# Kernel tuning notes

Measured on AMD Instinct MI355X. Metric: run time of the kernel, lower is better.

Reference implementation:

```python
import jax, jax.numpy as jnp
import numpy as np
import math

L, H, P = 16384, 128, 256


def setup_inputs() -> dict:
    key = jax.random.key(0)
    k = jax.random.split(key, 6)
    return {
        "input_sequence": jax.random.normal(k[0], (L, H), dtype=jnp.float32),
        "A_diag": jax.random.uniform(k[1], (P,), dtype=jnp.float32),
        "B": (jax.random.uniform(k[2], (P, H, 2), dtype=jnp.float32) * 2.0 - 1.0) / math.sqrt(H),
        "C": (jax.random.uniform(k[3], (H, P, 2), dtype=jnp.float32) * 2.0 - 1.0) / math.sqrt(P),
        "D": jax.random.normal(k[4], (H,), dtype=jnp.float32),
        "steps": jax.random.uniform(k[5], (P,), dtype=jnp.float32),
    }


def _binop(qi, qj):
    # 2x2 block-diagonal matrix product + affine state propagation, per channel.
    iA, iB, iC, iD, ib1, ib2 = qi
    jA, jB, jC, jD, jb1, jb2 = qj
    return (
        jA * iA + jB * iC,
        jA * iB + jB * iD,
        jC * iA + jD * iC,
        jC * iB + jD * iD,
        jA * ib1 + jB * ib2 + jb1,
        jC * ib1 + jD * ib2 + jb2,
    )


def reference(input_sequence, A_diag, B, C, D, steps):
    # LinOSS-IM discretization (implicit)
    A = jax.nn.relu(A_diag)                      # (P,)
    dt = jax.nn.sigmoid(steps)                   # (P,)
    Bc = B[..., 0] + 1j * B[..., 1]              # (P,H) complex64
    Cc = C[..., 0] + 1j * C[..., 1]              # (H,P) complex64

    Bu = input_sequence @ Bc.T                   # (L,P) complex64

    schur = 1.0 / (1.0 + dt ** 2 * A)
    M11 = 1.0 - dt ** 2 * A * schur
    M12 = -dt * A * schur
    M21 = dt * schur
    M22 = schur

    ones = jnp.ones((input_sequence.shape[0], A.shape[0]), dtype=input_sequence.dtype)
    F1 = M11 * Bu * dt                           # (L,P) complex
    F2 = M21 * Bu * dt

    elems = (M11 * ones, M12 * ones, M21 * ones, M22 * ones, F1, F2)
    _, _, _, _, _, x2 = jax.lax.associative_scan(_binop, elems)  # scan over L

    ys = jnp.real(x2 @ Cc.T)                     # (L,H)
    return ys + input_sequence * D
```

## Files before the change

### kernel.cpp

```cpp
#include <hip/hip_runtime.h>
#include <math.h>

#define L 16384
#define H 128
#define P 256
#define CL 32
#define NCH (L/CL)
#define GS 16
#define NG (NCH/GS)
#define KDIM 512
#define NBU 512

#define SENT 0xFFC0DEADFFC0DEADULL
#define SENT_WORDS (2*NCH*P + 2*NG*P)

typedef __attribute__((ext_vector_type(8))) short short8;
typedef __attribute__((ext_vector_type(4))) float f32x4;

__device__ inline unsigned short f2bf(float f){
  union { float f; unsigned u; } v; v.f = f;
  unsigned u = v.u;
  u += 0x7fffu + ((u >> 16) & 1u);
  return (unsigned short)(u >> 16);
}
__device__ inline float bf2f(unsigned short s){
  union { unsigned u; float f; } v; v.u = ((unsigned)s) << 16;
  return v.f;
}

struct Params { float M11,M12,M21,M22,s1,s2; };

__device__ inline Params get_params(const float* A_diag, const float* steps, int p){
  float A = A_diag[p]; A = A > 0.f ? A : 0.f;
  float dt = 1.f/(1.f + expf(-steps[p]));
  float schur = 1.f/(1.f + dt*dt*A);
  Params q;
  q.M11 = 1.f - dt*dt*A*schur;
  q.M12 = -dt*A*schur;
  q.M21 = dt*schur;
  q.M22 = schur;
  q.s1 = q.M11*dt;
  q.s2 = q.M21*dt;
  return q;
}

__device__ inline unsigned long long aload(const unsigned long long* p){
  return __hip_atomic_load((unsigned long long*)p, __ATOMIC_RELAXED,
                           __HIP_MEMORY_SCOPE_AGENT);
}
__device__ inline void apub(unsigned long long* p, unsigned long long v){
  (void)__hip_atomic_exchange(p, v, __ATOMIC_RELAXED, __HIP_MEMORY_SCOPE_AGENT);
}

__global__ __launch_bounds__(512) void prep_w(const float* __restrict__ B,
                                              const float* __restrict__ Cw,
                                              unsigned short* __restrict__ BWswz,
                                              unsigned short* __restrict__ Bswz,
                                              unsigned long long* __restrict__ sent){
  int gidx = blockIdx.x*512 + threadIdx.x;
  sent[gidx] = SENT;
  if (gidx < H*NBU){
    int k = gidx >> 9, n = gidx & 511;
    int p = n & 255, c2 = n >> 8;
    float v = B[((size_t)p*H + k)*2 + c2];
    BWswz[((size_t)(k>>3)*NBU + n)*8 + (k&7)] = f2bf(v);
  } else if (gidx < 2*H*NBU){
    int g2 = gidx - H*NBU;
    int k = g2 >> 7, n = g2 & 127;
    float v = (k < P) ? Cw[((size_t)n*P + k)*2]
                      : -Cw[((size_t)n*P + (k-P))*2 + 1];
    Bswz[((size_t)(k>>3)*H + n)*8 + (k&7)] = f2bf(v);
  }
}

__global__ __launch_bounds__(512, 4) void linoss_fused(
    const float* __restrict__ in,
    const float* __restrict__ A_diag,
    const float* __restrict__ steps,
    const float* __restrict__ Dv,
    const unsigned short* __restrict__ BWswz,
    const unsigned short* __restrict__ Bswz,
    unsigned long long* __restrict__ finals,
    unsigned long long* __restrict__ gfin,
    float* __restrict__ out)
{
  __shared__ unsigned short sX[CL][NBU+8];
  const int c   = blockIdx.x;
  const int tid = threadIdx.x;

  {
    int lane = tid & 63, w = tid >> 6;
    int ml = lane & 15, quad = lane >> 4;
    int mt = w & 1, ng = w >> 1;
    int lm0 = mt*16;
    const float* aptr = in + (size_t)(c*CL + lm0 + ml)*H + quad*8;
    short8 av[4];
    #pragma unroll
    for (int ks=0; ks<4; ks++){
      float4 f0 = *(const float4*)(aptr + ks*32);
      float4 f1 = *(const float4*)(aptr + ks*32 + 4);
      union { short8 s; unsigned short u[8]; } o;
      o.u[0]=f2bf(f0.x); o.u[1]=f2bf(f0.y); o.u[2]=f2bf(f0.z); o.u[3]=f2bf(f0.w);
      o.u[4]=f2bf(f1.x); o.u[5]=f2bf(f1.y); o.u[6]=f2bf(f1.z); o.u[7]=f2bf(f1.w);
      av[ks] = o.s;
    }
    f32x4 acc[8];
    #pragma unroll
    for (int t=0;t<8;t++) acc[t] = (f32x4){0.f,0.f,0.f,0.f};
    #pragma unroll
    for (int ks=0; ks<4; ks++){
      #pragma unroll
      for (int t=0;t<8;t++){
        int n0 = (ng*8 + t)*16;
        short8 bv = *(const short8*)(BWswz + ((size_t)(ks*4+quad)*NBU + n0 + ml)*8);
        acc[t] = __builtin_amdgcn_mfma_f32_16x16x32_bf16(av[ks], bv, acc[t], 0, 0, 0);
      }
    }
    #pragma unroll
    for (int t=0;t<8;t++){
      int n = (ng*8+t)*16 + ml;
      #pragma unroll
      for (int r=0;r<4;r++)
        sX[lm0 + quad*4 + r][n] = f2bf(acc[t][r]);
    }
  }
  __syncthreads();

  const int p = tid & 255, part = tid >> 8;
  Params q = get_params(A_diag, steps, p);
  float Ta=q.M11, Tb=q.M12, Tc=q.M21, Td=q.M22;
  #pragma unroll
  for (int s=0;s<5;s++){
    float na=Ta*Ta+Tb*Tc, nb=Ta*Tb+Tb*Td, nc=Tc*Ta+Td*Tc, nd=Tc*Tb+Td*Td;
    Ta=na;Tb=nb;Tc=nc;Td=nd;
  }
  float fx1=0.f, fx2=0.f;
  {
    #pragma unroll
    for (int i=0;i<CL;i++){
      float u = bf2f(sX[i][part*256 + p]);
      float n1 = q.M11*fx1 + q.M12*fx2 + q.s1*u;
      float n2 = q.M21*fx1 + q.M22*fx2 + q.s2*u;
      fx1 = n1; fx2 = n2;
    }
    union { unsigned long long u; float2 f; } w; w.f = make_float2(fx1,fx2);
    apub(&finals[(size_t)(part*NCH + c)*P + p], w.u);
  }

  const int g = c >> 4, iw = c & (GS-1);
  const unsigned long long* Fp = finals + (size_t)part*NCH*P + (size_t)g*GS*P + p;

  float z1=0.f, z2v=0.f;
  bool have_z = false;
  if (iw == GS-1){
    unsigned long long v[GS-1];
    #pragma unroll
    for (int j=0;j<GS-1;j++) v[j] = aload(Fp + (size_t)j*P);
    #pragma unroll
    for (int j=0;j<GS-1;j++){
      while (v[j]==SENT){ __builtin_amdgcn_s_sleep(2); v[j] = aload(Fp + (size_t)j*P); }
    }
    #pragma unroll
    for (int j=0;j<GS-1;j++){
      union { unsigned long long u; float2 f; } w; w.u = v[j];
      float n1 = Ta*z1 + Tb*z2v + w.f.x;
      float n2 = Tc*z1 + Td*z2v + w.f.y;
      z1=n1; z2v=n2;
    }
    have_z = true;
    float t1 = Ta*z1 + Tb*z2v + fx1;
    float t2 = Tc*z1 + Td*z2v + fx2;
    union { unsigned long long u; float2 f; } w; w.f = make_float2(t1,t2);
    apub(&gfin[(size_t)(part*NG + g)*P + p], w.u);
  }

  {
    float sa=1.f, sb=0.f, sc=0.f, sd=1.f;
    {
      float wa=Ta, wb=Tb, wc=Tc, wd=Td;
      #pragma unroll
      for (int bit=0; bit<4; bit++){
        if ((iw>>bit)&1){
          float na = wa*sa + wb*sc, nb = wa*sb + wb*sd;
          float nc = wc*sa + wd*sc, nd = wc*sb + wd*sd;
          sa=na; sb=nb; sc=nc; sd=nd;
        }
        float qa = wa*wa + wb*wc, qb = wa*wb + wb*wd;
        float qc = wc*wa + wd*wc, qd = wc*wb + wd*wd;
        wa=qa; wb=qb; wc=qc; wd=qd;
      }
    }
    float ga=Ta, gb=Tb, gc=Tc, gd=Td;
    #pragma unroll
    for (int s=0;s<4;s++){
      float na=ga*ga+gb*gc, nb=ga*gb+gb*gd, nc=gc*ga+gd*gc, nd=gc*gb+gd*gd;
      ga=na;gb=nb;gc=nc;gd=nd;
    }
    float y1=0.f, y2=0.f;
    {
      const unsigned long long* Gp = gfin + (size_t)part*NG*P + p;
      for (int t0=0; t0<NG-1 && t0<g; t0+=8){
        unsigned long long v[8];
        #pragma unroll
        for (int j=0;j<8;j++){
          int jj = t0+j;
          v[j] = (jj < g) ? aload(Gp + (size_t)jj*P) : 0ULL;
        }
        #pragma unroll
        for (int j=0;j<8;j++){
          int jj = t0+j;
          if (jj < g){
            while (v[j]==SENT){ __builtin_amdgcn_s_sleep(2); v[j] = aload(Gp + (size_t)jj*P); }
          }
        }
        #pragma unroll
        for (int j=0;j<8;j++){
          int jj = t0+j;
          if (jj < g){
            union { unsigned long long u; float2 f; } w; w.u = v[j];
            float n1 = ga*y1 + gb*y2 + w.f.x;
            float n2 = gc*y1 + gd*y2 + w.f.y;
            y1=n1; y2=n2;
          }
        }
      }
    }
    if (!have_z){
      for (int t0=0; t0<GS-1 && t0<iw; t0+=8){
        unsigned long long v[8];
        #pragma unroll
        for (int j=0;j<8;j++){
          int jj = t0+j;
          v[j] = (jj < iw) ? aload(Fp + (size_t)jj*P) : 0ULL;
        }
        #pragma unroll
        for (int j=0;j<8;j++){
          int jj = t0+j;
          if (jj < iw){
            while (v[j]==SENT){ __builtin_amdgcn_s_sleep(2); v[j] = aload(Fp + (size_t)jj*P); }
          }
        }
        #pragma unroll
        for (int j=0;j<8;j++){
          int jj = t0+j;
          if (jj < iw){
            union { unsigned long long u; float2 f; } w; w.u = v[j];
            float n1 = Ta*z1 + Tb*z2v + w.f.x;
            float n2 = Tc*z1 + Td*z2v + w.f.y;
            z1=n1; z2v=n2;
          }
        }
      }
    }
    float x1 = sa*y1 + sb*y2 + z1;
    float x2 = sc*y1 + sd*y2 + z2v;
    #pragma unroll
    for (int i=0;i<CL;i++){
      float u = bf2f(sX[i][part*256 + p]);
      float n1 = q.M11*x1 + q.M12*x2 + q.s1*u;
      float n2 = q.M21*x1 + q.M22*x2 + q.s2*u;
      x1 = n1; x2 = n2;
      sX[i][part*256 + p] = f2bf(x2);
    }
  }
  __syncthreads();

  {
    int lane = tid & 63, w = tid >> 6;
    int ml = lane & 15, quad = lane >> 4;
    int mt = w & 1;
    int ntb = (w >> 1) * 2;
    f32x4 acc[2];
    acc[0] = (f32x4){0.f,0.f,0.f,0.f};
    acc[1] = (f32x4){0.f,0.f,0.f,0.f};
    for (int ks=0; ks<KDIM/32; ks++){
      short8 av = *(const short8*)&sX[mt*16 + ml][ks*32 + quad*8];
      #pragma unroll
      for (int j=0;j<2;j++){
        short8 bv = *(const short8*)(Bswz + ((size_t)(ks*4+quad)*H + (ntb+j)*16 + ml)*8);
        acc[j] = __builtin_amdgcn_mfma_f32_16x16x32_bf16(av, bv, acc[j], 0, 0, 0);
      }
    }
    #pragma unroll
    for (int j=0;j<2;j++){
      int h = (ntb+j)*16 + ml;
      float dv = Dv[h];
      #pragma unroll
      for (int r=0;r<4;r++){
        int l = c*CL + mt*16 + quad*4 + r;
        out[(size_t)l*H + h] = acc[j][r] + in[(size_t)l*H + h]*dv;
      }
    }
  }
}

extern "C" void kernel_launch(void* const* d_in, const int* in_sizes, int n_in,
                              void* d_out, int out_size, void* d_ws, size_t ws_size,
                              hipStream_t stream) {
  const float* in     = (const float*)d_in[0];
  const float* A_diag = (const float*)d_in[1];
  const float* B      = (const float*)d_in[2];
  const float* Cw     = (const float*)d_in[3];
  const float* Dv     = (const float*)d_in[4];
  const float* steps  = (const float*)d_in[5];
  float* out = (float*)d_out;

  unsigned short* BWswz = (unsigned short*)d_ws;
  unsigned short* Bswz  = BWswz + (size_t)H*NBU;
  unsigned long long* finals = (unsigned long long*)(Bswz + (size_t)KDIM*H);
  unsigned long long* gfin   = finals + (size_t)2*NCH*P;

  prep_w<<<SENT_WORDS/512, 512, 0, stream>>>(B, Cw, BWswz, Bswz, finals);
  linoss_fused<<<NCH, 512, 0, stream>>>(in, A_diag, steps, Dv, BWswz, Bswz,
                                        finals, gfin, out);
}
```

Baseline: 98.22 us.

## Replace per-element sentinel polling with per-block ready flags for chunk carries

Cross-block carry propagation used to poll every published 64-bit value until it stopped equalling a sentinel, which required prep_w to fill every finals/gfin slot with the sentinel. Now each block drains its stores, syncs, and sets one ready flag per chunk and per group. Consumers wait on those flags with a few threads, then read the values in plain loads. This shrinks prep_w's initialization work and replaces many scattered per-element polls with a few flag polls, at the cost of extra __syncthreads and store drains on the critical path.

```diff
diff --git a/kernel.cpp b/kernel.cpp
--- a/kernel.cpp
+++ b/kernel.cpp
@@ -10,9 +10,6 @@
 #define NG (NCH/GS)
 #define KDIM 512
 #define NBU 512
-
-#define SENT 0xFFC0DEADFFC0DEADULL
-#define SENT_WORDS (2*NCH*P + 2*NG*P)
 
 typedef __attribute__((ext_vector_type(8))) short short8;
 typedef __attribute__((ext_vector_type(4))) float f32x4;
@@ -51,20 +48,27 @@
 __device__ inline void apub(unsigned long long* p, unsigned long long v){
   (void)__hip_atomic_exchange(p, v, __ATOMIC_RELAXED, __HIP_MEMORY_SCOPE_AGENT);
 }
+__device__ inline void fpub(unsigned* p){
+  (void)__hip_atomic_exchange(p, 1u, __ATOMIC_RELAXED, __HIP_MEMORY_SCOPE_AGENT);
+}
+__device__ inline void wait_flag(unsigned* f){
+  while (__hip_atomic_load(f, __ATOMIC_RELAXED, __HIP_MEMORY_SCOPE_AGENT) == 0u)
+    __builtin_amdgcn_s_sleep(2);
+}
 
 __global__ __launch_bounds__(512) void prep_w(const float* __restrict__ B,
                                               const float* __restrict__ Cw,
                                               unsigned short* __restrict__ BWswz,
                                               unsigned short* __restrict__ Bswz,
-                                              unsigned long long* __restrict__ sent){
+                                              unsigned* __restrict__ flags){
   int gidx = blockIdx.x*512 + threadIdx.x;
-  sent[gidx] = SENT;
+  if (gidx < NCH + NG) flags[gidx] = 0u;
   if (gidx < H*NBU){
     int k = gidx >> 9, n = gidx & 511;
     int p = n & 255, c2 = n >> 8;
     float v = B[((size_t)p*H + k)*2 + c2];
     BWswz[((size_t)(k>>3)*NBU + n)*8 + (k&7)] = f2bf(v);
-  } else if (gidx < 2*H*NBU){
+  } else {
     int g2 = gidx - H*NBU;
     int k = g2 >> 7, n = g2 & 127;
     float v = (k < P) ? Cw[((size_t)n*P + k)*2]
@@ -82,6 +86,8 @@
     const unsigned short* __restrict__ Bswz,
     unsigned long long* __restrict__ finals,
     unsigned long long* __restrict__ gfin,
+    unsigned* __restrict__ flag1,
+    unsigned* __restrict__ flag2,
     float* __restrict__ out)
 {
   __shared__ unsigned short sX[CL][NBU+8];
@@ -146,6 +152,9 @@
     union { unsigned long long u; float2 f; } w; w.f = make_float2(fx1,fx2);
     apub(&finals[(size_t)(part*NCH + c)*P + p], w.u);
   }
+  asm volatile("s_waitcnt vmcnt(0)" ::: "memory");
+  __syncthreads();
+  if (tid == 0) fpub(&flag1[c]);
 
   const int g = c >> 4, iw = c & (GS-1);
   const unsigned long long* Fp = finals + (size_t)part*NCH*P + (size_t)g*GS*P + p;
@@ -153,13 +162,11 @@
   float z1=0.f, z2v=0.f;
   bool have_z = false;
   if (iw == GS-1){
+    if (tid < GS-1) wait_flag(&flag1[g*GS + tid]);
+    __syncthreads();
     unsigned long long v[GS-1];
     #pragma unroll
     for (int j=0;j<GS-1;j++) v[j] = aload(Fp + (size_t)j*P);
-    #pragma unroll
-    for (int j=0;j<GS-1;j++){
-      while (v[j]==SENT){ __builtin_amdgcn_s_sleep(2); v[j] = aload(Fp + (size_t)j*P); }
-    }
     #pragma unroll
     for (int j=0;j<GS-1;j++){
       union { unsigned long long u; float2 f; } w; w.u = v[j];
@@ -172,46 +179,47 @@
     float t2 = Tc*z1 + Td*z2v + fx2;
     union { unsigned long long u; float2 f; } w; w.f = make_float2(t1,t2);
     apub(&gfin[(size_t)(part*NG + g)*P + p], w.u);
-  }
-
-  {
-    float sa=1.f, sb=0.f, sc=0.f, sd=1.f;
-    {
-      float wa=Ta, wb=Tb, wc=Tc, wd=Td;
-      #pragma unroll
-      for (int bit=0; bit<4; bit++){
-        if ((iw>>bit)&1){
-          float na = wa*sa + wb*sc, nb = wa*sb + wb*sd;
-          float nc = wc*sa + wd*sc, nd = wc*sb + wd*sd;
-          sa=na; sb=nb; sc=nc; sd=nd;
-        }
-        float qa = wa*wa + wb*wc, qb = wa*wb + wb*wd;
-        float qc = wc*wa + wd*wc, qd = wc*wb + wd*wd;
-        wa=qa; wb=qb; wc=qc; wd=qd;
-      }
-    }
-    float ga=Ta, gb=Tb, gc=Tc, gd=Td;
-    #pragma unroll
-    for (int s=0;s<4;s++){
-      float na=ga*ga+gb*gc, nb=ga*gb+gb*gd, nc=gc*ga+gd*gc, nd=gc*gb+gd*gd;
-      ga=na;gb=nb;gc=nc;gd=nd;
-    }
+    asm volatile("s_waitcnt vmcnt(0)" ::: "memory");
+    __syncthreads();
+    if (tid == 0) fpub(&flag2[g]);
+  }
+
+  float sa=1.f, sb=0.f, sc=0.f, sd=1.f;
+  {
+    float wa=Ta, wb=Tb, wc=Tc, wd=Td;
+    #pragma unroll
+    for (int bit=0; bit<4; bit++){
+      if ((iw>>bit)&1){
+        float na = wa*sa + wb*sc, nb = wa*sb + wb*sd;
+        float nc = wc*sa + wd*sc, nd = wc*sb + wd*sd;
+        sa=na; sb=nb; sc=nc; sd=nd;
+      }
+      float qa = wa*wa + wb*wc, qb = wa*wb + wb*wd;
+      float qc = wc*wa + wd*wc, qd = wc*wb + wd*wd;
+      wa=qa; wb=qb; wc=qc; wd=qd;
+    }
+  }
+  float ga=Ta, gb=Tb, gc=Tc, gd=Td;
+  #pragma unroll
+  for (int s=0;s<4;s++){
+    float na=ga*ga+gb*gc, nb=ga*gb+gb*gd, nc=gc*ga+gd*gc, nd=gc*gb+gd*gd;
+    ga=na;gb=nb;gc=nc;gd=nd;
+  }
+
+  if (tid < g)                             wait_flag(&flag2[tid]);
+  if (!have_z && tid >= 64 && tid < 64+iw) wait_flag(&flag1[g*GS + (tid-64)]);
+  __syncthreads();
+
+  {
     float y1=0.f, y2=0.f;
     {
       const unsigned long long* Gp = gfin + (size_t)part*NG*P + p;
-      for (int t0=0; t0<NG-1 && t0<g; t0+=8){
+      for (int t0=0; t0<g; t0+=8){
         unsigned long long v[8];
         #pragma unroll
         for (int j=0;j<8;j++){
           int jj = t0+j;
           v[j] = (jj < g) ? aload(Gp + (size_t)jj*P) : 0ULL;
-        }
-        #pragma unroll
-        for (int j=0;j<8;j++){
-          int jj = t0+j;
-          if (jj < g){
-            while (v[j]==SENT){ __builtin_amdgcn_s_sleep(2); v[j] = aload(Gp + (size_t)jj*P); }
-          }
         }
         #pragma unroll
         for (int j=0;j<8;j++){
@@ -226,19 +234,12 @@
       }
     }
     if (!have_z){
-      for (int t0=0; t0<GS-1 && t0<iw; t0+=8){
+      for (int t0=0; t0<iw; t0+=8){
         unsigned long long v[8];
         #pragma unroll
         for (int j=0;j<8;j++){
           int jj = t0+j;
           v[j] = (jj < iw) ? aload(Fp + (size_t)jj*P) : 0ULL;
-        }
-        #pragma unroll
-        for (int j=0;j<8;j++){
-          int jj = t0+j;
-          if (jj < iw){
-            while (v[j]==SENT){ __builtin_amdgcn_s_sleep(2); v[j] = aload(Fp + (size_t)jj*P); }
-          }
         }
         #pragma unroll
         for (int j=0;j<8;j++){
@@ -309,8 +310,11 @@
   unsigned short* Bswz  = BWswz + (size_t)H*NBU;
   unsigned long long* finals = (unsigned long long*)(Bswz + (size_t)KDIM*H);
   unsigned long long* gfin   = finals + (size_t)2*NCH*P;
-
-  prep_w<<<SENT_WORDS/512, 512, 0, stream>>>(B, Cw, BWswz, Bswz, finals);
+  unsigned* flags = (unsigned*)(gfin + (size_t)2*NG*P);
+  unsigned* flag1 = flags;
+  unsigned* flag2 = flags + NCH;
+
+  prep_w<<<256, 512, 0, stream>>>(B, Cw, BWswz, Bswz, flags);
   linoss_fused<<<NCH, 512, 0, stream>>>(in, A_diag, steps, Dv, BWswz, Bswz,
-                                        finals, gfin, out);
-}
+                                        finals, gfin, flag1, flag2, out);
+}
```

Result: slower. 100.5 us (+2.3%).

## Replace spin-wait decoupled lookback with separate kernels for chunk, group and output passes

Applied to the files above, without the earlier changes.

The single fused kernel used sentinel-initialized buffers and atomic spin-waits so chunks could publish their final states and read their predecessors' states. The new version splits this into three launches: per-chunk final states, a small per-group combine kernel, and an output kernel that recomputes the Bu GEMM and reads the completed states with plain loads. This removes the sentinel fill and the spin polling, but adds two kernel launches and recomputes the input projection GEMM a second time. Chunk inputs are also cached in registers, and the state writes to LDS are batched.

```diff
diff --git a/kernel.cpp b/kernel.cpp
--- a/kernel.cpp
+++ b/kernel.cpp
@@ -10,9 +10,6 @@
 #define NG (NCH/GS)
 #define KDIM 512
 #define NBU 512
-
-#define SENT 0xFFC0DEADFFC0DEADULL
-#define SENT_WORDS (2*NCH*P + 2*NG*P)
 
 typedef __attribute__((ext_vector_type(8))) short short8;
 typedef __attribute__((ext_vector_type(4))) float f32x4;
@@ -44,27 +41,57 @@
   return q;
 }
 
-__device__ inline unsigned long long aload(const unsigned long long* p){
-  return __hip_atomic_load((unsigned long long*)p, __ATOMIC_RELAXED,
-                           __HIP_MEMORY_SCOPE_AGENT);
-}
-__device__ inline void apub(unsigned long long* p, unsigned long long v){
-  (void)__hip_atomic_exchange(p, v, __ATOMIC_RELAXED, __HIP_MEMORY_SCOPE_AGENT);
+__device__ inline void chunk_bu_to_lds(int c, const float* __restrict__ in,
+                                       const unsigned short* __restrict__ BWswz,
+                                       unsigned short (*sBu)[NBU+8]){
+  int tid = threadIdx.x;
+  int lane = tid & 63, w = tid >> 6;
+  int ml = lane & 15, quad = lane >> 4;
+  int mt = w & 1, ng = w >> 1;
+  int lm0 = mt*16;
+  const float* aptr = in + (size_t)(c*CL + lm0 + ml)*H + quad*8;
+  short8 av[4];
+  #pragma unroll
+  for (int ks=0; ks<4; ks++){
+    float4 f0 = *(const float4*)(aptr + ks*32);
+    float4 f1 = *(const float4*)(aptr + ks*32 + 4);
+    union { short8 s; unsigned short u[8]; } o;
+    o.u[0]=f2bf(f0.x); o.u[1]=f2bf(f0.y); o.u[2]=f2bf(f0.z); o.u[3]=f2bf(f0.w);
+    o.u[4]=f2bf(f1.x); o.u[5]=f2bf(f1.y); o.u[6]=f2bf(f1.z); o.u[7]=f2bf(f1.w);
+    av[ks] = o.s;
+  }
+  f32x4 acc[8];
+  #pragma unroll
+  for (int t=0;t<8;t++) acc[t] = (f32x4){0.f,0.f,0.f,0.f};
+  #pragma unroll
+  for (int ks=0; ks<4; ks++){
+    #pragma unroll
+    for (int t=0;t<8;t++){
+      int n0 = (ng*8 + t)*16;
+      short8 bv = *(const short8*)(BWswz + ((size_t)(ks*4+quad)*NBU + n0 + ml)*8);
+      acc[t] = __builtin_amdgcn_mfma_f32_16x16x32_bf16(av[ks], bv, acc[t], 0, 0, 0);
+    }
+  }
+  #pragma unroll
+  for (int t=0;t<8;t++){
+    int n = (ng*8+t)*16 + ml;
+    #pragma unroll
+    for (int r=0;r<4;r++)
+      sBu[lm0 + quad*4 + r][n] = f2bf(acc[t][r]);
+  }
 }
 
 __global__ __launch_bounds__(512) void prep_w(const float* __restrict__ B,
                                               const float* __restrict__ Cw,
                                               unsigned short* __restrict__ BWswz,
-                                              unsigned short* __restrict__ Bswz,
-                                              unsigned long long* __restrict__ sent){
+                                              unsigned short* __restrict__ Bswz){
   int gidx = blockIdx.x*512 + threadIdx.x;
-  sent[gidx] = SENT;
   if (gidx < H*NBU){
     int k = gidx >> 9, n = gidx & 511;
     int p = n & 255, c2 = n >> 8;
     float v = B[((size_t)p*H + k)*2 + c2];
     BWswz[((size_t)(k>>3)*NBU + n)*8 + (k&7)] = f2bf(v);
-  } else if (gidx < 2*H*NBU){
+  } else {
     int g2 = gidx - H*NBU;
     int k = g2 >> 7, n = g2 & 127;
     float v = (k < P) ? Cw[((size_t)n*P + k)*2]
@@ -73,60 +100,83 @@
   }
 }
 
-__global__ __launch_bounds__(512, 4) void linoss_fused(
+__global__ __launch_bounds__(512, 4) void k1_bu(
+    const float* __restrict__ in,
+    const float* __restrict__ A_diag,
+    const float* __restrict__ steps,
+    const unsigned short* __restrict__ BWswz,
+    float* __restrict__ finals)
+{
+  __shared__ unsigned short sBu[CL][NBU+8];
+  const int c   = blockIdx.x;
+  const int tid = threadIdx.x;
+  chunk_bu_to_lds(c, in, BWswz, sBu);
+  __syncthreads();
+
+  const int p = tid & 255, part = tid >> 8;
+  Params q = get_params(A_diag, steps, p);
+  float u[CL];
+  #pragma unroll
+  for (int i=0;i<CL;i++) u[i] = bf2f(sBu[i][part*256 + p]);
+  float fx1=0.f, fx2=0.f;
+  #pragma unroll
+  for (int i=0;i<CL;i++){
+    float n1 = q.M11*fx1 + q.M12*fx2 + q.s1*u[i];
+    float n2 = q.M21*fx1 + q.M22*fx2 + q.s2*u[i];
+    fx1 = n1; fx2 = n2;
+  }
+  ((float2*)finals)[(size_t)(part*NCH + c)*P + p] = make_float2(fx1,fx2);
+}
+
+__global__ __launch_bounds__(512) void k15_grp(
+    const float* __restrict__ A_diag,
+    const float* __restrict__ steps,
+    const float* __restrict__ finals,
+    float* __restrict__ gfin)
+{
+  const int g = blockIdx.x;
+  const int tid = threadIdx.x;
+  const int p = tid & 255, part = tid >> 8;
+  Params q = get_params(A_diag, steps, p);
+  float Ta=q.M11, Tb=q.M12, Tc=q.M21, Td=q.M22;
+  #pragma unroll
+  for (int s=0;s<5;s++){
+    float na=Ta*Ta+Tb*Tc, nb=Ta*Tb+Tb*Td, nc=Tc*Ta+Td*Tc, nd=Tc*Tb+Td*Td;
+    Ta=na;Tb=nb;Tc=nc;Td=nd;
+  }
+  const float2* F = (const float2*)finals + (size_t)part*NCH*P + (size_t)g*GS*P + p;
+  float2 v[GS];
+  #pragma unroll
+  for (int j=0;j<GS;j++) v[j] = F[(size_t)j*P];
+  float x1=0.f, x2=0.f;
+  #pragma unroll
+  for (int j=0;j<GS;j++){
+    float n1 = Ta*x1 + Tb*x2 + v[j].x;
+    float n2 = Tc*x1 + Td*x2 + v[j].y;
+    x1=n1; x2=n2;
+  }
+  ((float2*)gfin)[(size_t)(part*NG + g)*P + p] = make_float2(x1,x2);
+}
+
+__global__ __launch_bounds__(512, 4) void k2_out(
     const float* __restrict__ in,
     const float* __restrict__ A_diag,
     const float* __restrict__ steps,
     const float* __restrict__ Dv,
     const unsigned short* __restrict__ BWswz,
     const unsigned short* __restrict__ Bswz,
-    unsigned long long* __restrict__ finals,
-    unsigned long long* __restrict__ gfin,
+    const float* __restrict__ finals,
+    const float* __restrict__ gfin,
     float* __restrict__ out)
 {
   __shared__ unsigned short sX[CL][NBU+8];
   const int c   = blockIdx.x;
   const int tid = threadIdx.x;
-
-  {
-    int lane = tid & 63, w = tid >> 6;
-    int ml = lane & 15, quad = lane >> 4;
-    int mt = w & 1, ng = w >> 1;
-    int lm0 = mt*16;
-    const float* aptr = in + (size_t)(c*CL + lm0 + ml)*H + quad*8;
-    short8 av[4];
-    #pragma unroll
-    for (int ks=0; ks<4; ks++){
-      float4 f0 = *(const float4*)(aptr + ks*32);
-      float4 f1 = *(const float4*)(aptr + ks*32 + 4);
-      union { short8 s; unsigned short u[8]; } o;
-      o.u[0]=f2bf(f0.x); o.u[1]=f2bf(f0.y); o.u[2]=f2bf(f0.z); o.u[3]=f2bf(f0.w);
-      o.u[4]=f2bf(f1.x); o.u[5]=f2bf(f1.y); o.u[6]=f2bf(f1.z); o.u[7]=f2bf(f1.w);
-      av[ks] = o.s;
-    }
-    f32x4 acc[8];
-    #pragma unroll
-    for (int t=0;t<8;t++) acc[t] = (f32x4){0.f,0.f,0.f,0.f};
-    #pragma unroll
-    for (int ks=0; ks<4; ks++){
-      #pragma unroll
-      for (int t=0;t<8;t++){
-        int n0 = (ng*8 + t)*16;
-        short8 bv = *(const short8*)(BWswz + ((size_t)(ks*4+quad)*NBU + n0 + ml)*8);
-        acc[t] = __builtin_amdgcn_mfma_f32_16x16x32_bf16(av[ks], bv, acc[t], 0, 0, 0);
-      }
-    }
-    #pragma unroll
-    for (int t=0;t<8;t++){
-      int n = (ng*8+t)*16 + ml;
-      #pragma unroll
-      for (int r=0;r<4;r++)
-        sX[lm0 + quad*4 + r][n] = f2bf(acc[t][r]);
-    }
-  }
+  chunk_bu_to_lds(c, in, BWswz, sX);
   __syncthreads();
 
   const int p = tid & 255, part = tid >> 8;
+  const int g = c >> 4, iw = c & (GS-1);
   Params q = get_params(A_diag, steps, p);
   float Ta=q.M11, Tb=q.M12, Tc=q.M21, Td=q.M22;
   #pragma unroll
@@ -134,135 +184,88 @@
     float na=Ta*Ta+Tb*Tc, nb=Ta*Tb+Tb*Td, nc=Tc*Ta+Td*Tc, nd=Tc*Tb+Td*Td;
     Ta=na;Tb=nb;Tc=nc;Td=nd;
   }
-  float fx1=0.f, fx2=0.f;
+
+  float u[CL];
+  #pragma unroll
+  for (int i=0;i<CL;i++) u[i] = bf2f(sX[i][part*256 + p]);
+
+  float sa=1.f, sb=0.f, sc=0.f, sd=1.f;
   {
+    float wa=Ta, wb=Tb, wc=Tc, wd=Td;
     #pragma unroll
-    for (int i=0;i<CL;i++){
-      float u = bf2f(sX[i][part*256 + p]);
-      float n1 = q.M11*fx1 + q.M12*fx2 + q.s1*u;
-      float n2 = q.M21*fx1 + q.M22*fx2 + q.s2*u;
-      fx1 = n1; fx2 = n2;
-    }
-    union { unsigned long long u; float2 f; } w; w.f = make_float2(fx1,fx2);
-    apub(&finals[(size_t)(part*NCH + c)*P + p], w.u);
-  }
-
-  const int g = c >> 4, iw = c & (GS-1);
-  const unsigned long long* Fp = finals + (size_t)part*NCH*P + (size_t)g*GS*P + p;
-
+    for (int bit=0; bit<4; bit++){
+      if ((iw>>bit)&1){
+        float na = wa*sa + wb*sc, nb = wa*sb + wb*sd;
+        float nc = wc*sa + wd*sc, nd = wc*sb + wd*sd;
+        sa=na; sb=nb; sc=nc; sd=nd;
+      }
+      float qa = wa*wa + wb*wc, qb = wa*wb + wb*wd;
+      float qc = wc*wa + wd*wc, qd = wc*wb + wd*wd;
+      wa=qa; wb=qb; wc=qc; wd=qd;
+    }
+  }
+  float ga=Ta, gb=Tb, gc=Tc, gd=Td;
+  #pragma unroll
+  for (int s=0;s<4;s++){
+    float na=ga*ga+gb*gc, nb=ga*gb+gb*gd, nc=gc*ga+gd*gc, nd=gc*gb+gd*gd;
+    ga=na;gb=nb;gc=nc;gd=nd;
+  }
+
+  float y1=0.f, y2=0.f;
+  {
+    const float2* Gp = (const float2*)gfin + (size_t)part*NG*P + p;
+    for (int t0=0; t0<g; t0+=8){
+      float2 v[8];
+      #pragma unroll
+      for (int j=0;j<8;j++){
+        int jj = t0+j;
+        v[j] = (jj < g) ? Gp[(size_t)jj*P] : make_float2(0.f,0.f);
+      }
+      #pragma unroll
+      for (int j=0;j<8;j++){
+        int jj = t0+j;
+        if (jj < g){
+          float n1 = ga*y1 + gb*y2 + v[j].x;
+          float n2 = gc*y1 + gd*y2 + v[j].y;
+          y1=n1; y2=n2;
+        }
+      }
+    }
+  }
   float z1=0.f, z2v=0.f;
-  bool have_z = false;
-  if (iw == GS-1){
-    unsigned long long v[GS-1];
-    #pragma unroll
-    for (int j=0;j<GS-1;j++) v[j] = aload(Fp + (size_t)j*P);
-    #pragma unroll
-    for (int j=0;j<GS-1;j++){
-      while (v[j]==SENT){ __builtin_amdgcn_s_sleep(2); v[j] = aload(Fp + (size_t)j*P); }
-    }
-    #pragma unroll
-    for (int j=0;j<GS-1;j++){
-      union { unsigned long long u; float2 f; } w; w.u = v[j];
-      float n1 = Ta*z1 + Tb*z2v + w.f.x;
-      float n2 = Tc*z1 + Td*z2v + w.f.y;
-      z1=n1; z2v=n2;
-    }
-    have_z = true;
-    float t1 = Ta*z1 + Tb*z2v + fx1;
-    float t2 = Tc*z1 + Td*z2v + fx2;
-    union { unsigned long long u; float2 f; } w; w.f = make_float2(t1,t2);
-    apub(&gfin[(size_t)(part*NG + g)*P + p], w.u);
-  }
-
   {
-    float sa=1.f, sb=0.f, sc=0.f, sd=1.f;
-    {
-      float wa=Ta, wb=Tb, wc=Tc, wd=Td;
-      #pragma unroll
-      for (int bit=0; bit<4; bit++){
-        if ((iw>>bit)&1){
-          float na = wa*sa + wb*sc, nb = wa*sb + wb*sd;
-          float nc = wc*sa + wd*sc, nd = wc*sb + wd*sd;
-          sa=na; sb=nb; sc=nc; sd=nd;
+    const float2* Fp = (const float2*)finals + (size_t)part*NCH*P + (size_t)g*GS*P + p;
+    for (int t0=0; t0<iw; t0+=8){
+      float2 v[8];
+      #pragma unroll
+      for (int j=0;j<8;j++){
+        int jj = t0+j;
+        v[j] = (jj < iw) ? Fp[(size_t)jj*P] : make_float2(0.f,0.f);
+      }
+      #pragma unroll
+      for (int j=0;j<8;j++){
+        int jj = t0+j;
+        if (jj < iw){
+          float n1 = Ta*z1 + Tb*z2v + v[j].x;
+          float n2 = Tc*z1 + Td*z2v + v[j].y;
+          z1=n1; z2v=n2;
         }
-        float qa = wa*wa + wb*wc, qb = wa*wb + wb*wd;
-        float qc = wc*wa + wd*wc, qd = wc*wb + wd*wd;
-        wa=qa; wb=qb; wc=qc; wd=qd;
-      }
-    }
-    float ga=Ta, gb=Tb, gc=Tc, gd=Td;
-    #pragma unroll
-    for (int s=0;s<4;s++){
-      float na=ga*ga+gb*gc, nb=ga*gb+gb*gd, nc=gc*ga+gd*gc, nd=gc*gb+gd*gd;
-      ga=na;gb=nb;gc=nc;gd=nd;
-    }
-    float y1=0.f, y2=0.f;
-    {
-      const unsigned long long* Gp = gfin + (size_t)part*NG*P + p;
-      for (int t0=0; t0<NG-1 && t0<g; t0+=8){
-        unsigned long long v[8];
-        #pragma unroll
-        for (int j=0;j<8;j++){
-          int jj = t0+j;
-          v[j] = (jj < g) ? aload(Gp + (size_t)jj*P) : 0ULL;
-        }
-        #pragma unroll
-        for (int j=0;j<8;j++){
-          int jj = t0+j;
-          if (jj < g){
-            while (v[j]==SENT){ __builtin_amdgcn_s_sleep(2); v[j] = aload(Gp + (size_t)jj*P); }
-          }
-        }
-        #pragma unroll
-        for (int j=0;j<8;j++){
-          int jj = t0+j;
-          if (jj < g){
-            union { unsigned long long u; float2 f; } w; w.u = v[j];
-            float n1 = ga*y1 + gb*y2 + w.f.x;
-            float n2 = gc*y1 + gd*y2 + w.f.y;
-            y1=n1; y2=n2;
-          }
-        }
-      }
-    }
-    if (!have_z){
-      for (int t0=0; t0<GS-1 && t0<iw; t0+=8){
-        unsigned long long v[8];
-        #pragma unroll
-        for (int j=0;j<8;j++){
-          int jj = t0+j;
-          v[j] = (jj < iw) ? aload(Fp + (size_t)jj*P) : 0ULL;
-        }
-        #pragma unroll
-        for (int j=0;j<8;j++){
-          int jj = t0+j;
-          if (jj < iw){
-            while (v[j]==SENT){ __builtin_amdgcn_s_sleep(2); v[j] = aload(Fp + (size_t)jj*P); }
-          }
-        }
-        #pragma unroll
-        for (int j=0;j<8;j++){
-          int jj = t0+j;
-          if (jj < iw){
-            union { unsigned long long u; float2 f; } w; w.u = v[j];
-            float n1 = Ta*z1 + Tb*z2v + w.f.x;
-            float n2 = Tc*z1 + Td*z2v + w.f.y;
-            z1=n1; z2v=n2;
-          }
-        }
-      }
-    }
-    float x1 = sa*y1 + sb*y2 + z1;
-    float x2 = sc*y1 + sd*y2 + z2v;
-    #pragma unroll
-    for (int i=0;i<CL;i++){
-      float u = bf2f(sX[i][part*256 + p]);
-      float n1 = q.M11*x1 + q.M12*x2 + q.s1*u;
-      float n2 = q.M21*x1 + q.M22*x2 + q.s2*u;
-      x1 = n1; x2 = n2;
-      sX[i][part*256 + p] = f2bf(x2);
-    }
-  }
+      }
+    }
+  }
+  float x1 = sa*y1 + sb*y2 + z1;
+  float x2 = sc*y1 + sd*y2 + z2v;
+
+  unsigned short hw[CL];
+  #pragma unroll
+  for (int i=0;i<CL;i++){
+    float n1 = q.M11*x1 + q.M12*x2 + q.s1*u[i];
+    float n2 = q.M21*x1 + q.M22*x2 + q.s2*u[i];
+    x1 = n1; x2 = n2;
+    hw[i] = f2bf(x2);
+  }
+  #pragma unroll
+  for (int i=0;i<CL;i++) sX[i][part*256 + p] = hw[i];
   __syncthreads();
 
   {
@@ -307,10 +310,12 @@
 
   unsigned short* BWswz = (unsigned short*)d_ws;
   unsigned short* Bswz  = BWswz + (size_t)H*NBU;
-  unsigned long long* finals = (unsigned long long*)(Bswz + (size_t)KDIM*H);
-  unsigned long long* gfin   = finals + (size_t)2*NCH*P;
-
-  prep_w<<<SENT_WORDS/512, 512, 0, stream>>>(B, Cw, BWswz, Bswz, finals);
-  linoss_fused<<<NCH, 512, 0, stream>>>(in, A_diag, steps, Dv, BWswz, Bswz,
-                                        finals, gfin, out);
-}
+  float* finals = (float*)(Bswz + (size_t)KDIM*H);
+  float* gfin   = finals + (size_t)2*NCH*P*2;
+
+  prep_w <<<256, 512, 0, stream>>>(B, Cw, BWswz, Bswz);
+  k1_bu  <<<NCH, 512, 0, stream>>>(in, A_diag, steps, BWswz, finals);
+  k15_grp<<<NG,  512, 0, stream>>>(A_diag, steps, finals, gfin);
+  k2_out <<<NCH, 512, 0, stream>>>(in, A_diag, steps, Dv, BWswz, Bswz,
+                                   finals, gfin, out);
+}
```

Result: slower. 108.4 us (+10.4%).
